# Kernel tuning notes

Measured on AMD Instinct MI355X. Metric: run time of the kernel, lower is better.

Reference implementation:

```python
import jax, jax.numpy as jnp
import numpy as np

VOCAB = 32000
DIM = 1024
DFF = 4096
NLLM = 3
B, S = 2, 2048
THRESH = 0.98
EPS = 1e-8


def setup_inputs() -> dict:
    key = jax.random.key(0)
    ks = jax.random.split(key, 5)
    x = jax.random.randint(ks[0], (B, S), 0, VOCAB)
    emb = 0.02 * jax.random.normal(ks[1], (VOCAB, DIM), jnp.float32)
    ln_g = jnp.ones((NLLM, DIM), jnp.float32)
    ln_b = jnp.zeros((NLLM, DIM), jnp.float32)
    W1 = 0.002 * jax.random.normal(ks[2], (NLLM, DIM, DFF), jnp.float32)
    b1 = jnp.zeros((NLLM, DFF), jnp.float32)
    W2 = 0.002 * jax.random.normal(ks[3], (NLLM, DFF, DIM), jnp.float32)
    b2 = jnp.zeros((NLLM, DIM), jnp.float32)
    W_out = (1.0 / np.sqrt(DIM)) * jax.random.normal(ks[4], (VOCAB, DIM), jnp.float32)
    return dict(x=x, emb=emb, ln_g=ln_g, ln_b=ln_b, W1=W1, b1=b1, W2=W2, b2=b2, W_out=W_out)


def _layernorm(h, g, b):
    m = jnp.mean(h, axis=-1, keepdims=True)
    v = jnp.var(h, axis=-1, keepdims=True)
    return (h - m) * jax.lax.rsqrt(v + 1e-5) * g + b


def reference(x, emb, ln_g, ln_b, W1, b1, W2, b2, W_out):
    # Cascaded early-exit ensemble. The torch code physically re-packs surviving
    # tokens; since each LLM block here is per-token (residual MLP), a masked
    # formulation computes identical per-token math and is jit-compatible.
    Bb, Ss = x.shape
    T = Bb * Ss
    h = emb[x.reshape(T)]                      # [T, D] token embeddings
    active = jnp.ones((T,), dtype=bool)
    final = jnp.zeros((T, VOCAB), dtype=h.dtype)
    for i in range(NLLM):                      # fixed, small number of LLMs
        hn = _layernorm(h, ln_g[i], ln_b[i])
        mlp = jax.nn.gelu(hn @ W1[i] + b1[i]) @ W2[i] + b2[i]
        h_out = h + mlp                        # [T, D]
        logits = h_out @ W_out.T               # [T, V] shared output head
        cos = jnp.sum(h * h_out, axis=-1) / (
            jnp.linalg.norm(h, axis=-1) * jnp.linalg.norm(h_out, axis=-1) + EPS)
        is_last = (i == NLLM - 1)
        should_exit = cos >= THRESH
        take = active if is_last else (active & should_exit)
        final = jnp.where(take[:, None], logits, final)   # scatter logits for exiting tokens
        active = active & (~take)
        h = jnp.where(active[:, None], h_out, h)          # continuing tokens carry h_out forward
    return final.reshape(Bb, Ss, VOCAB)
```

## Files before the change

### kernel.cpp

```cpp
#include <hip/hip_runtime.h>
#include <hip/hip_bf16.h>
#include <stdint.h>

constexpr int TK   = 4096;
constexpr int DIMC = 1024;
constexpr int DFFC = 4096;
constexpr int VOC  = 32000;
constexpr int NL   = 3;

typedef __attribute__((ext_vector_type(8))) short bf16x8;
typedef __attribute__((ext_vector_type(8))) _Float16 half8;
typedef __attribute__((ext_vector_type(4))) float f32x4;
using u16 = unsigned short;

__device__ __forceinline__ u16 f2bf(float f) {
  unsigned int u = __float_as_uint(f);
  u += 0x7FFF + ((u >> 16) & 1);
  return (u16)(u >> 16);
}

__device__ __forceinline__ void split16(float v, u16& hi, u16& lo) {
  _Float16 a = (_Float16)v;
  _Float16 b = (_Float16)(v - (float)a);
  hi = __builtin_bit_cast(u16, a);
  lo = __builtin_bit_cast(u16, b);
}

__device__ __forceinline__ float gelu_f(float x) {
  float x3 = x * x * x;
  return 0.5f * x * (1.0f + tanhf(0.7978845608028654f * (x + 0.044715f * x3)));
}

__device__ __forceinline__ void gll16(const void* g, void* l) {
  __builtin_amdgcn_global_load_lds(
      (const __attribute__((address_space(1))) unsigned int*)g,
      (__attribute__((address_space(3))) unsigned int*)l, 16, 0, 0);
}

__global__ __launch_bounds__(256) void k_init(const int* __restrict__ x,
    const float* __restrict__ emb, float* __restrict__ h,
    int* __restrict__ surv, int* __restrict__ cnts) {
  const int t = blockIdx.x, tid = threadIdx.x;
  if (t == 0 && tid < 16) cnts[tid] = (tid == 12) ? TK : 0;
  if (tid == 0) surv[t] = t;
  const int tok = x[t];
  ((float4*)(h + (size_t)t * DIMC))[tid] =
      ((const float4*)(emb + (size_t)tok * DIMC))[tid];
}

__global__ __launch_bounds__(256) void k_ln(const float* __restrict__ h,
    const int* __restrict__ surv, const int* __restrict__ pM,
    const float* __restrict__ g, const float* __restrict__ b,
    u16* __restrict__ hn1, u16* __restrict__ hn2) {
  const int bidx = blockIdx.x;
  if (bidx >= *pM) return;
  const int t = surv[bidx];
  const int tid = threadIdx.x;
  const int lane = tid & 63, wid = tid >> 6;
  __shared__ float sm[4];
  float4 v = ((const float4*)(h + (size_t)t * DIMC))[tid];
  float s = v.x + v.y + v.z + v.w;
#pragma unroll
  for (int o = 32; o; o >>= 1) s += __shfl_down(s, o);
  if (lane == 0) sm[wid] = s;
  __syncthreads();
  const float mean = (sm[0] + sm[1] + sm[2] + sm[3]) * (1.0f / DIMC);
  __syncthreads();
  float4 d;
  d.x = v.x - mean; d.y = v.y - mean; d.z = v.z - mean; d.w = v.w - mean;
  float q = d.x * d.x + d.y * d.y + d.z * d.z + d.w * d.w;
#pragma unroll
  for (int o = 32; o; o >>= 1) q += __shfl_down(q, o);
  if (lane == 0) sm[wid] = q;
  __syncthreads();
  const float var = (sm[0] + sm[1] + sm[2] + sm[3]) * (1.0f / DIMC);
  const float rstd = 1.0f / sqrtf(var + 1e-5f);
  float4 gg = ((const float4*)g)[tid];
  float4 bb = ((const float4*)b)[tid];
  float o4[4];
  o4[0] = (d.x * rstd * gg.x + bb.x) * 16.f;
  o4[1] = (d.y * rstd * gg.y + bb.y) * 16.f;
  o4[2] = (d.z * rstd * gg.z + bb.z) * 16.f;
  o4[3] = (d.w * rstd * gg.w + bb.w) * 16.f;
  ushort4 u1, u2;
  split16(o4[0], u1.x, u2.x); split16(o4[1], u1.y, u2.y);
  split16(o4[2], u1.z, u2.z); split16(o4[3], u1.w, u2.w);
  ((ushort4*)(hn1 + (size_t)bidx * DIMC))[tid] = u1;
  ((ushort4*)(hn2 + (size_t)bidx * DIMC))[tid] = u2;
}

__global__ __launch_bounds__(256) void k_splitw(const float* __restrict__ W,
    int K, int N, u16* __restrict__ O1, u16* __restrict__ O2) {
  __shared__ float t[64][65];
  const int bk = blockIdx.x * 64, bn = blockIdx.y * 64;
  const int lx = threadIdx.x & 63, ly = threadIdx.x >> 6;
#pragma unroll
  for (int i = 0; i < 64; i += 4)
    t[ly + i][lx] = W[(size_t)(bk + ly + i) * N + bn + lx];
  __syncthreads();
  const int n4 = threadIdx.x >> 4;
  const int kq = (threadIdx.x & 15) * 4;
#pragma unroll
  for (int j = 0; j < 4; ++j) {
    const int n = j * 16 + n4;
    ushort4 h1, h2;
    {
      float v0 = t[kq + 0][n] * 256.f, v1 = t[kq + 1][n] * 256.f;
      float v2 = t[kq + 2][n] * 256.f, v3 = t[kq + 3][n] * 256.f;
      split16(v0, h1.x, h2.x); split16(v1, h1.y, h2.y);
      split16(v2, h1.z, h2.z); split16(v3, h1.w, h2.w);
    }
    const size_t o = (size_t)(bn + n) * K + bk + kq;
    *(ushort4*)&O1[o] = h1;
    *(ushort4*)&O2[o] = h2;
  }
}

__global__ __launch_bounds__(256) void k_cvtb(const float* __restrict__ in,
    u16* __restrict__ o, int n4) {
  int i = blockIdx.x * blockDim.x + threadIdx.x;
  const int stride = gridDim.x * blockDim.x;
  for (; i < n4; i += stride) {
    float4 v = ((const float4*)in)[i];
    ushort4 u;
    u.x = f2bf(v.x); u.y = f2bf(v.y); u.z = f2bf(v.z); u.w = f2bf(v.w);
    ((ushort4*)o)[i] = u;
  }
}

__global__ __launch_bounds__(512, 1) void k_mlp1(
    const u16* __restrict__ wsb,
    int offA, int pstrA,
    int offB, int pstrB,
    const int* __restrict__ pM,
    const float* __restrict__ bias,
    u16* __restrict__ O1, u16* __restrict__ O2)
{
  const int x = blockIdx.x & 7, g = blockIdx.x >> 3;
  const int rb = g & 15;
  const int cb = x * 2 + (g >> 4);
  const int M = *pM;
  if (rb * 256 >= M) return;
  const int n0 = cb * 256;

  __shared__ u16 S[2][32768];
  const int tid = threadIdx.x, w = tid >> 6, l = tid & 63;
  const int lr16 = l & 15, hi = l >> 4;

  int goff[8];
#pragma unroll
  for (int q = 0; q < 8; ++q) {
    const int bi = w * 8 + q;
    const int side = bi >> 5;
    const int pl = (bi >> 4) & 1;
    const int j = bi & 15;
    const int row = (side ? n0 : rb * 256) + j * 16 + lr16;
    const int base = side ? (offB + pl * pstrB) : (offA + pl * pstrA);
    goff[q] = base + row * DIMC + hi * 8;
  }

  const int wr = w >> 2, wc = w & 3;
  f32x4 acc[8][4];
#pragma unroll
  for (int mi = 0; mi < 8; ++mi)
#pragma unroll
    for (int ni = 0; ni < 4; ++ni) acc[mi][ni] = (f32x4){0.f, 0.f, 0.f, 0.f};

  auto STAGE = [&](int buf, int kt) {
#pragma unroll
    for (int q = 0; q < 8; ++q)
      gll16(wsb + (size_t)(goff[q] + kt * 32), (void*)&S[buf][(w * 8 + q) * 512]);
  };

  STAGE(0, 0);
  STAGE(1, 1);
  const int NT = DIMC / 32;
  for (int kt = 0; kt < NT; ++kt) {
    const int cur = kt & 1;
    if (kt + 1 < NT) asm volatile("s_waitcnt vmcnt(8)" ::: "memory");
    else             asm volatile("s_waitcnt vmcnt(0)" ::: "memory");
    __builtin_amdgcn_s_barrier();
    half8 b1v[4], b2v[4];
#pragma unroll
    for (int ni = 0; ni < 4; ++ni) {
      const int sub = (32 + wc * 4 + ni) * 512 + l * 8;
      b1v[ni] = *(const half8*)&S[cur][sub];
      b2v[ni] = *(const half8*)&S[cur][sub + 8192];
    }
#pragma unroll
    for (int mh = 0; mh < 2; ++mh) {
      half8 a1v[4], a2v[4];
#pragma unroll
      for (int i = 0; i < 4; ++i) {
        const int sub = (wr * 8 + mh * 4 + i) * 512 + l * 8;
        a1v[i] = *(const half8*)&S[cur][sub];
        a2v[i] = *(const half8*)&S[cur][sub + 8192];
      }
      __builtin_amdgcn_s_setprio(1);
#pragma unroll
      for (int i = 0; i < 4; ++i)
#pragma unroll
        for (int ni = 0; ni < 4; ++ni) {
          f32x4 c = acc[mh * 4 + i][ni];
          c = __builtin_amdgcn_mfma_f32_16x16x32_f16(a2v[i], b1v[ni], c, 0, 0, 0);
          c = __builtin_amdgcn_mfma_f32_16x16x32_f16(a1v[i], b2v[ni], c, 0, 0, 0);
          c = __builtin_amdgcn_mfma_f32_16x16x32_f16(a1v[i], b1v[ni], c, 0, 0, 0);
          acc[mh * 4 + i][ni] = c;
        }
      __builtin_amdgcn_s_setprio(0);
    }
    asm volatile("s_waitcnt lgkmcnt(0)" ::: "memory");
    __builtin_amdgcn_s_barrier();
    if (kt + 2 < NT) STAGE(cur, kt + 2);
  }

#pragma unroll
  for (int mi = 0; mi < 8; ++mi)
#pragma unroll
    for (int ni = 0; ni < 4; ++ni) {
      const int n = n0 + wc * 64 + ni * 16 + lr16;
#pragma unroll
      for (int r = 0; r < 4; ++r) {
        const int m = rb * 256 + wr * 128 + mi * 16 + hi * 4 + r;
        float v = gelu_f(acc[mi][ni][r] * (1.f / 4096.f) + bias[n]) * 64.f;
        u16 h1, h2; split16(v, h1, h2);
        O1[(size_t)m * DFFC + n] = h1;
        O2[(size_t)m * DFFC + n] = h2;
      }
    }
}

__global__ __launch_bounds__(512, 1) void k_mlp2(
    const u16* __restrict__ wsb,
    int offA, int pstrA,
    int offB, int pstrB,
    const int* __restrict__ pM,
    float* __restrict__ PO)
{
  const int x = blockIdx.x & 7, g = blockIdx.x >> 3;
  const int rb = g & 15;
  const int cz = x * 2 + (g >> 4);
  const int cb = cz & 7, z = cz >> 3;
  const int M = *pM;
  if (rb * 256 >= M) return;
  const int n0 = cb * 128;
  const int kz = z * 2048;

  __shared__ u16 S[2][24576];
  const int tid = threadIdx.x, w = tid >> 6, l = tid & 63;
  const int lr16 = l & 15, hi = l >> 4;

  int goff[6];
#pragma unroll
  for (int q = 0; q < 6; ++q) {
    const int bi = w * 6 + q;
    int base, row;
    if (bi < 32) {
      const int pl = bi >> 4, j = bi & 15;
      base = offA + pl * pstrA;
      row = rb * 256 + j * 16 + lr16;
    } else {
      const int bb = bi - 32, pl = bb >> 3, j = bb & 7;
      base = offB + pl * pstrB;
      row = n0 + j * 16 + lr16;
    }
    goff[q] = base + row * DFFC + kz + hi * 8;
  }

  const int wr = w >> 1, wc = w & 1;
  f32x4 acc[4][4];
#pragma unroll
  for (int mi = 0; mi < 4; ++mi)
#pragma unroll
    for (int ni = 0; ni < 4; ++ni) acc[mi][ni] = (f32x4){0.f, 0.f, 0.f, 0.f};

  auto STAGE = [&](int buf, int kt) {
#pragma unroll
    for (int q = 0; q < 6; ++q)
      gll16(wsb + (size_t)(goff[q] + kt * 32), (void*)&S[buf][(w * 6 + q) * 512]);
  };

  STAGE(0, 0);
  STAGE(1, 1);
  const int NT = 2048 / 32;
  for (int kt = 0; kt < NT; ++kt) {
    const int cur = kt & 1;
    if (kt + 1 < NT) asm volatile("s_waitcnt vmcnt(6)" ::: "memory");
    else             asm volatile("s_waitcnt vmcnt(0)" ::: "memory");
    __builtin_amdgcn_s_barrier();
    half8 a1v[4], a2v[4], b1v[4], b2v[4];
#pragma unroll
    for (int mi = 0; mi < 4; ++mi) {
      const int sub = (wr * 4 + mi) * 512 + l * 8;
      a1v[mi] = *(const half8*)&S[cur][sub];
      a2v[mi] = *(const half8*)&S[cur][sub + 8192];
    }
#pragma unroll
    for (int ni = 0; ni < 4; ++ni) {
      const int sub = (32 + wc * 4 + ni) * 512 + l * 8;
      b1v[ni] = *(const half8*)&S[cur][sub];
      b2v[ni] = *(const half8*)&S[cur][sub + 4096];
    }
    __builtin_amdgcn_s_setprio(1);
#pragma unroll
    for (int mi = 0; mi < 4; ++mi)
#pragma unroll
      for (int ni = 0; ni < 4; ++ni) {
        f32x4 c = acc[mi][ni];
        c = __builtin_amdgcn_mfma_f32_16x16x32_f16(a2v[mi], b1v[ni], c, 0, 0, 0);
        c = __builtin_amdgcn_mfma_f32_16x16x32_f16(a1v[mi], b2v[ni], c, 0, 0, 0);
        c = __builtin_amdgcn_mfma_f32_16x16x32_f16(a1v[mi], b1v[ni], c, 0, 0, 0);
        acc[mi][ni] = c;
      }
    __builtin_amdgcn_s_setprio(0);
    asm volatile("s_waitcnt lgkmcnt(0)" ::: "memory");
    __builtin_amdgcn_s_barrier();
    if (kt + 2 < NT) STAGE(cur, kt + 2);
  }

#pragma unroll
  for (int mi = 0; mi < 4; ++mi)
#pragma unroll
    for (int ni = 0; ni < 4; ++ni) {
      const int n = n0 + wc * 64 + ni * 16 + lr16;
#pragma unroll
      for (int r = 0; r < 4; ++r) {
        const int m = rb * 256 + wr * 64 + mi * 16 + hi * 4 + r;
        PO[(size_t)(z * TK + m) * DIMC + n] = acc[mi][ni][r] * (1.f / 16384.f);
      }
    }
}

__global__ __launch_bounds__(256) void k_decide(
    float* __restrict__ h, const float* __restrict__ p,
    const float* __restrict__ bias,
    const int* __restrict__ surv_in, int* __restrict__ surv_out,
    const int* __restrict__ pM, int* __restrict__ cnts,
    int* __restrict__ exit_idx, u16* __restrict__ hexit,
    int stage)
{
  const int bidx = blockIdx.x;
  if (bidx >= *pM) return;
  const int t = surv_in[bidx];
  const int tid = threadIdx.x;
  const int lane = tid & 63, wid = tid >> 6;
  __shared__ float sm[12];
  __shared__ int sif[2];
  float4 a  = ((const float4*)(h + (size_t)t * DIMC))[tid];
  float4 p0 = ((const float4*)(p + (size_t)bidx * DIMC))[tid];
  float4 p1 = ((const float4*)(p + (size_t)(TK + bidx) * DIMC))[tid];
  float4 bb = ((const float4*)bias)[tid];
  float4 o;
  o.x = a.x + p0.x + p1.x + bb.x;
  o.y = a.y + p0.y + p1.y + bb.y;
  o.z = a.z + p0.z + p1.z + bb.z;
  o.w = a.w + p0.w + p1.w + bb.w;
  float hh = a.x * a.x + a.y * a.y + a.z * a.z + a.w * a.w;
  float ho = a.x * o.x + a.y * o.y + a.z * o.z + a.w * o.w;
  float oo = o.x * o.x + o.y * o.y + o.z * o.z + o.w * o.w;
#pragma unroll
  for (int off = 32; off; off >>= 1) {
    hh += __shfl_down(hh, off);
    ho += __shfl_down(ho, off);
    oo += __shfl_down(oo, off);
  }
  if (lane == 0) { sm[wid] = hh; sm[4 + wid] = ho; sm[8 + wid] = oo; }
  __syncthreads();
  if (tid == 0) {
    int take;
    if (stage == NL - 1) take = 1;
    else {
      const float HH = sm[0] + sm[1] + sm[2] + sm[3];
      const float HO = sm[4] + sm[5] + sm[6] + sm[7];
      const float OO = sm[8] + sm[9] + sm[10] + sm[11];
      const float cosv = HO / (sqrtf(HH) * sqrtf(OO) + 1e-8f);
      take = (cosv >= 0.98f) ? 1 : 0;
    }
    int pos;
    if (take) {
      pos = atomicAdd(&cnts[stage], 1);
      exit_idx[pos] = t;
    } else {
      pos = atomicAdd(&cnts[4 + stage], 1);
      surv_out[pos] = t;
    }
    sif[0] = take; sif[1] = pos;
  }
  __syncthreads();
  if (sif[0]) {
    u16* dst = hexit + (size_t)sif[1] * DIMC;
    ushort4 u;
    u.x = f2bf(o.x); u.y = f2bf(o.y); u.z = f2bf(o.z); u.w = f2bf(o.w);
    ((ushort4*)dst)[tid] = u;
  } else {
    ((float4*)(h + (size_t)t * DIMC))[tid] = o;
  }
}

__global__ __launch_bounds__(512, 4) void k_logits(
    const u16* __restrict__ wsb, int offA, int offB,
    const int* __restrict__ pcnt,
    const int* __restrict__ exit_idx,
    float* __restrict__ out)
{
  const int x = blockIdx.x & 7, g = blockIdx.x >> 3;
  const int rb = g & 15;
  const int cb = x * 32 + (g >> 4);
  if (cb >= VOC / 128) return;
  const int cnt = *pcnt;
  if (rb * 256 >= cnt) return;
  const int n0 = cb * 128;

  __shared__ u16 S[2][12288];
  const int tid = threadIdx.x, w = tid >> 6, l = tid & 63;
  const int lr16 = l & 15, hi = l >> 4;

  int goff[3], loff[3];
#pragma unroll
  for (int q = 0; q < 3; ++q) {
    const int bi = w * 3 + q;
    if (bi < 16) {
      goff[q] = offA + (rb * 256 + bi * 16 + lr16) * DIMC + hi * 8;
      loff[q] = bi * 512;
    } else {
      const int j = bi - 16;
      goff[q] = offB + (n0 + j * 16 + lr16) * DIMC + hi * 8;
      loff[q] = 8192 + j * 512;
    }
  }

  const int wr = w >> 1, wc = w & 1;
  f32x4 acc[4][4];
#pragma unroll
  for (int mi = 0; mi < 4; ++mi)
#pragma unroll
    for (int ni = 0; ni < 4; ++ni) acc[mi][ni] = (f32x4){0.f, 0.f, 0.f, 0.f};

  auto STAGE = [&](int buf, int kt) {
#pragma unroll
    for (int q = 0; q < 3; ++q)
      gll16(wsb + (size_t)(goff[q] + kt * 32), (void*)&S[buf][loff[q]]);
  };

  STAGE(0, 0);
  STAGE(1, 1);
  const int NT = DIMC / 32;
  for (int kt = 0; kt < NT; ++kt) {
    const int cur = kt & 1;
    if (kt + 1 < NT) asm volatile("s_waitcnt vmcnt(3)" ::: "memory");
    else             asm volatile("s_waitcnt vmcnt(0)" ::: "memory");
    __builtin_amdgcn_s_barrier();
    bf16x8 aF[4], bF[4];
#pragma unroll
    for (int mi = 0; mi < 4; ++mi)
      aF[mi] = *(const bf16x8*)&S[cur][(wr * 4 + mi) * 512 + l * 8];
#pragma unroll
    for (int ni = 0; ni < 4; ++ni)
      bF[ni] = *(const bf16x8*)&S[cur][8192 + (wc * 4 + ni) * 512 + l * 8];
    __builtin_amdgcn_s_setprio(1);
#pragma unroll
    for (int mi = 0; mi < 4; ++mi)
#pragma unroll
      for (int ni = 0; ni < 4; ++ni)
        acc[mi][ni] = __builtin_amdgcn_mfma_f32_16x16x32_bf16(aF[mi], bF[ni], acc[mi][ni], 0, 0, 0);
    __builtin_amdgcn_s_setprio(0);
    asm volatile("s_waitcnt lgkmcnt(0)" ::: "memory");
    __builtin_amdgcn_s_barrier();
    if (kt + 2 < NT) STAGE(cur, kt + 2);
  }

  const int mvalid = cnt - rb * 256;
#pragma unroll
  for (int mi = 0; mi < 4; ++mi)
#pragma unroll
    for (int r = 0; r < 4; ++r) {
      const int mrow = wr * 64 + mi * 16 + hi * 4 + r;
      if (mrow < mvalid) {
        const int tok = exit_idx[rb * 256 + mrow];
        float* orow = out + (size_t)tok * VOC + n0 + wc * 64 + lr16;
#pragma unroll
        for (int ni = 0; ni < 4; ++ni)
          __builtin_nontemporal_store(acc[mi][ni][r], &orow[ni * 16]);
      }
    }
}

extern "C" void kernel_launch(void* const* d_in, const int* in_sizes, int n_in,
                              void* d_out, int out_size, void* d_ws, size_t ws_size,
                              hipStream_t stream)
{
  const int*   x    = (const int*)d_in[0];
  const float* emb  = (const float*)d_in[1];
  const float* ln_g = (const float*)d_in[2];
  const float* ln_b = (const float*)d_in[3];
  const float* W1   = (const float*)d_in[4];
  const float* b1   = (const float*)d_in[5];
  const float* W2   = (const float*)d_in[6];
  const float* b2   = (const float*)d_in[7];
  const float* Wout = (const float*)d_in[8];
  float* out = (float*)d_out;

  char* p = (char*)d_ws;
  size_t off = 0;
  auto alloc = [&](size_t bytes) -> void* {
    void* r = p + off;
    off += (bytes + 255) & ~(size_t)255;
    return r;
  };
  u16* wsb = (u16*)d_ws;
  float* h    = (float*)alloc((size_t)TK * DIMC * 4);
  float* pbuf = (float*)alloc((size_t)2 * TK * DIMC * 4);
  u16* hn1 = (u16*)pbuf;
  u16* hn2 = hn1 + (size_t)TK * DIMC;
  u16* act1 = (u16*)alloc((size_t)2 * TK * DFFC * 2);
  u16* act2 = act1 + (size_t)TK * DFFC;
  u16* Woutb = (u16*)alloc((size_t)VOC * DIMC * 2);
  u16* Wt = (u16*)alloc((size_t)2 * DFFC * DIMC * 2);
  u16* hexit = (u16*)alloc((size_t)TK * DIMC * 2);
  int* exit_idx = (int*)alloc((size_t)TK * 4);
  int* surv_a   = (int*)alloc((size_t)TK * 4);
  int* surv_b   = (int*)alloc((size_t)TK * 4);
  int* cnts     = (int*)alloc(64 * 4);

  const int offHn  = (int)(hn1  - wsb);
  const int offAct = (int)(act1 - wsb);
  const int offWob = (int)(Woutb- wsb);
  const int offWt  = (int)(Wt   - wsb);
  const int offHex = (int)(hexit- wsb);
  const int pstrHn  = TK * DIMC;
  const int pstrAct = TK * DFFC;
  const int pstrW   = DFFC * DIMC;

  k_init<<<TK, 256, 0, stream>>>(x, emb, h, surv_a, cnts);
  k_cvtb<<<2048, 256, 0, stream>>>(Wout, Woutb, VOC * DIMC / 4);
  int* surv_in  = surv_a;
  int* surv_out = surv_b;
  for (int i = 0; i < NL; ++i) {
    const int* pM = (i == 0) ? (cnts + 12) : (cnts + 4 + (i - 1));
    k_ln<<<TK, 256, 0, stream>>>(h, surv_in, pM, ln_g + i * DIMC, ln_b + i * DIMC, hn1, hn2);
    k_splitw<<<dim3(DIMC / 64, DFFC / 64), 256, 0, stream>>>(
        W1 + (size_t)i * DIMC * DFFC, DIMC, DFFC, Wt, Wt + (size_t)DFFC * DIMC);
    k_mlp1<<<256, 512, 0, stream>>>(
        wsb, offHn, pstrHn, offWt, pstrW, pM, b1 + (size_t)i * DFFC, act1, act2);
    k_splitw<<<dim3(DFFC / 64, DIMC / 64), 256, 0, stream>>>(
        W2 + (size_t)i * DFFC * DIMC, DFFC, DIMC, Wt, Wt + (size_t)DIMC * DFFC);
    k_mlp2<<<256, 512, 0, stream>>>(
        wsb, offAct, pstrAct, offWt, pstrW, pM, pbuf);
    k_decide<<<TK, 256, 0, stream>>>(h, pbuf, b2 + (size_t)i * DIMC,
        surv_in, surv_out, pM, cnts, exit_idx, hexit, i);
    k_logits<<<4096, 512, 0, stream>>>(wsb, offHex, offWob, cnts + i, exit_idx, out);
    int* tmp = surv_in; surv_in = surv_out; surv_out = tmp;
  }
}
```

Baseline: 1.367 ms.

## Batch all weight splits into one launch and triple-buffer GEMM pipelines

All six per-layer W1/W2 fp16 hi/lo split-transpose conversions now run in a single up-front kernel that writes into per-layer weight buffers, replacing six small launches inside the layer loop. The mlp2 and logits GEMMs go from double to triple buffering in LDS, prefetching three K-tiles ahead with adjusted vmcnt waits to hide more global-load latency. This costs more workspace memory and more LDS per block, which may reduce occupancy for k_logits (launch bound 4 blocks/CU at 72KB).

```diff
diff --git a/kernel.cpp b/kernel.cpp
--- a/kernel.cpp
+++ b/kernel.cpp
@@ -89,10 +89,26 @@
   ((ushort4*)(hn2 + (size_t)bidx * DIMC))[tid] = u2;
 }
 
-__global__ __launch_bounds__(256) void k_splitw(const float* __restrict__ W,
-    int K, int N, u16* __restrict__ O1, u16* __restrict__ O2) {
+__global__ __launch_bounds__(256) void k_splitw_all(
+    const float* __restrict__ W1, const float* __restrict__ W2,
+    u16* __restrict__ W1all, u16* __restrict__ W2all)
+{
+  int bid = blockIdx.x;
+  const int s = bid >> 11; bid &= 2047;
+  const int tens = bid >> 10; bid &= 1023;
+  const float* W; int K, N; u16 *O1, *O2; int bk, bn;
+  if (tens == 0) {
+    W = W1 + (size_t)s * DIMC * DFFC; K = DIMC; N = DFFC;
+    O1 = W1all + (size_t)s * 2 * DFFC * DIMC;
+    O2 = O1 + (size_t)DFFC * DIMC;
+    bk = (bid & 15) * 64; bn = (bid >> 4) * 64;
+  } else {
+    W = W2 + (size_t)s * DFFC * DIMC; K = DFFC; N = DIMC;
+    O1 = W2all + (size_t)s * 2 * DIMC * DFFC;
+    O2 = O1 + (size_t)DIMC * DFFC;
+    bk = (bid >> 4) * 64; bn = (bid & 15) * 64;
+  }
   __shared__ float t[64][65];
-  const int bk = blockIdx.x * 64, bn = blockIdx.y * 64;
   const int lx = threadIdx.x & 63, ly = threadIdx.x >> 6;
 #pragma unroll
   for (int i = 0; i < 64; i += 4)
@@ -246,7 +262,7 @@
   const int n0 = cb * 128;
   const int kz = z * 2048;
 
-  __shared__ u16 S[2][24576];
+  __shared__ u16 S[3][24576];
   const int tid = threadIdx.x, w = tid >> 6, l = tid & 63;
   const int lr16 = l & 15, hi = l >> 4;
 
@@ -282,11 +298,13 @@
 
   STAGE(0, 0);
   STAGE(1, 1);
+  STAGE(2, 2);
   const int NT = 2048 / 32;
+  int cur = 0;
   for (int kt = 0; kt < NT; ++kt) {
-    const int cur = kt & 1;
-    if (kt + 1 < NT) asm volatile("s_waitcnt vmcnt(6)" ::: "memory");
-    else             asm volatile("s_waitcnt vmcnt(0)" ::: "memory");
+    if (kt + 2 < NT)      asm volatile("s_waitcnt vmcnt(12)" ::: "memory");
+    else if (kt + 1 < NT) asm volatile("s_waitcnt vmcnt(6)" ::: "memory");
+    else                  asm volatile("s_waitcnt vmcnt(0)" ::: "memory");
     __builtin_amdgcn_s_barrier();
     half8 a1v[4], a2v[4], b1v[4], b2v[4];
 #pragma unroll
@@ -315,7 +333,8 @@
     __builtin_amdgcn_s_setprio(0);
     asm volatile("s_waitcnt lgkmcnt(0)" ::: "memory");
     __builtin_amdgcn_s_barrier();
-    if (kt + 2 < NT) STAGE(cur, kt + 2);
+    if (kt + 3 < NT) STAGE(cur, kt + 3);
+    cur = (cur == 2) ? 0 : cur + 1;
   }
 
 #pragma unroll
@@ -411,7 +430,7 @@
   if (rb * 256 >= cnt) return;
   const int n0 = cb * 128;
 
-  __shared__ u16 S[2][12288];
+  __shared__ u16 S[3][12288];
   const int tid = threadIdx.x, w = tid >> 6, l = tid & 63;
   const int lr16 = l & 15, hi = l >> 4;
 
@@ -444,11 +463,13 @@
 
   STAGE(0, 0);
   STAGE(1, 1);
+  STAGE(2, 2);
   const int NT = DIMC / 32;
+  int cur = 0;
   for (int kt = 0; kt < NT; ++kt) {
-    const int cur = kt & 1;
-    if (kt + 1 < NT) asm volatile("s_waitcnt vmcnt(3)" ::: "memory");
-    else             asm volatile("s_waitcnt vmcnt(0)" ::: "memory");
+    if (kt + 2 < NT)      asm volatile("s_waitcnt vmcnt(6)" ::: "memory");
+    else if (kt + 1 < NT) asm volatile("s_waitcnt vmcnt(3)" ::: "memory");
+    else                  asm volatile("s_waitcnt vmcnt(0)" ::: "memory");
     __builtin_amdgcn_s_barrier();
     bf16x8 aF[4], bF[4];
 #pragma unroll
@@ -466,7 +487,8 @@
     __builtin_amdgcn_s_setprio(0);
     asm volatile("s_waitcnt lgkmcnt(0)" ::: "memory");
     __builtin_amdgcn_s_barrier();
-    if (kt + 2 < NT) STAGE(cur, kt + 2);
+    if (kt + 3 < NT) STAGE(cur, kt + 3);
+    cur = (cur == 2) ? 0 : cur + 1;
   }
 
   const int mvalid = cnt - rb * 256;
@@ -515,7 +537,8 @@
   u16* act1 = (u16*)alloc((size_t)2 * TK * DFFC * 2);
   u16* act2 = act1 + (size_t)TK * DFFC;
   u16* Woutb = (u16*)alloc((size_t)VOC * DIMC * 2);
-  u16* Wt = (u16*)alloc((size_t)2 * DFFC * DIMC * 2);
+  u16* W1all = (u16*)alloc((size_t)NL * 2 * DFFC * DIMC * 2);
+  u16* W2all = (u16*)alloc((size_t)NL * 2 * DIMC * DFFC * 2);
   u16* hexit = (u16*)alloc((size_t)TK * DIMC * 2);
   int* exit_idx = (int*)alloc((size_t)TK * 4);
   int* surv_a   = (int*)alloc((size_t)TK * 4);
@@ -525,7 +548,8 @@
   const int offHn  = (int)(hn1  - wsb);
   const int offAct = (int)(act1 - wsb);
   const int offWob = (int)(Woutb- wsb);
-  const int offWt  = (int)(Wt   - wsb);
+  const int offW1a = (int)(W1all- wsb);
+  const int offW2a = (int)(W2all- wsb);
   const int offHex = (int)(hexit- wsb);
   const int pstrHn  = TK * DIMC;
   const int pstrAct = TK * DFFC;
@@ -533,19 +557,17 @@
 
   k_init<<<TK, 256, 0, stream>>>(x, emb, h, surv_a, cnts);
   k_cvtb<<<2048, 256, 0, stream>>>(Wout, Woutb, VOC * DIMC / 4);
+  k_splitw_all<<<6144, 256, 0, stream>>>(W1, W2, W1all, W2all);
   int* surv_in  = surv_a;
   int* surv_out = surv_b;
   for (int i = 0; i < NL; ++i) {
     const int* pM = (i == 0) ? (cnts + 12) : (cnts + 4 + (i - 1));
     k_ln<<<TK, 256, 0, stream>>>(h, surv_in, pM, ln_g + i * DIMC, ln_b + i * DIMC, hn1, hn2);
-    k_splitw<<<dim3(DIMC / 64, DFFC / 64), 256, 0, stream>>>(
-        W1 + (size_t)i * DIMC * DFFC, DIMC, DFFC, Wt, Wt + (size_t)DFFC * DIMC);
     k_mlp1<<<256, 512, 0, stream>>>(
-        wsb, offHn, pstrHn, offWt, pstrW, pM, b1 + (size_t)i * DFFC, act1, act2);
-    k_splitw<<<dim3(DFFC / 64, DIMC / 64), 256, 0, stream>>>(
-        W2 + (size_t)i * DFFC * DIMC, DFFC, DIMC, Wt, Wt + (size_t)DIMC * DFFC);
+        wsb, offHn, pstrHn, offW1a + i * 2 * pstrW, pstrW,
+        pM, b1 + (size_t)i * DFFC, act1, act2);
     k_mlp2<<<256, 512, 0, stream>>>(
-        wsb, offAct, pstrAct, offWt, pstrW, pM, pbuf);
+        wsb, offAct, pstrAct, offW2a + i * 2 * pstrW, pstrW, pM, pbuf);
     k_decide<<<TK, 256, 0, stream>>>(h, pbuf, b2 + (size_t)i * DIMC,
         surv_in, surv_out, pM, cnts, exit_idx, hexit, i);
     k_logits<<<4096, 512, 0, stream>>>(wsb, offHex, offWob, cnts + i, exit_idx, out);
```

New measurement: 1.399 ms. +2.3%, slower.
